# Optimization experiments

Measured on AMD Instinct MI355X. Metric: run time of the kernel, lower is better.

The kernel has to match this reference:

```python
import jax, jax.numpy as jnp
import numpy as np

N_CHANNELS = 270
N_SUBJECTS = 200
B, T = 256, 1024


def setup_inputs() -> dict:
    key = jax.random.key(0)
    k_x, k_s = jax.random.split(key)
    x = jax.random.normal(k_x, (B, N_CHANNELS, T), dtype=jnp.float32)
    subjects = jax.random.randint(k_s, (B,), 0, N_SUBJECTS, dtype=jnp.int64)
    # init_id=True: weights start as identity, then divided by sqrt(C)
    weights = jnp.broadcast_to(jnp.eye(N_CHANNELS, dtype=jnp.float32),
                               (N_SUBJECTS, N_CHANNELS, N_CHANNELS)) / np.sqrt(N_CHANNELS)
    return {"x": x, "subjects": subjects, "weights": weights}


def reference(x, subjects, weights):
    # Gather per-sample CxC weight, then batched matmul: bct,bcd->bdt
    w = weights[subjects]  # (B, C, C)
    return jnp.einsum('bct,bcd->bdt', x, w)
```

## Files before the change

kernel.cpp:

```cpp
#include <hip/hip_runtime.h>


#define C_    270
#define T_    1024
#define B_    256
#define NSUB_ 200

#define BM 96
#define BN 128
#define BK 32
#define NK 9
#define ROWU32 20
#define BOFF (BM * ROWU32)
#define LDSU32 ((BM + BN) * ROWU32)

typedef __attribute__((ext_vector_type(8))) short bf16x8;
typedef __attribute__((ext_vector_type(4))) float f32x4;
typedef __attribute__((ext_vector_type(2))) float f32x2;
typedef __attribute__((ext_vector_type(2))) unsigned u32x2;

__device__ __forceinline__ unsigned pk(float lo, float hi) {
    unsigned a = __builtin_bit_cast(unsigned, lo);
    unsigned b = __builtin_bit_cast(unsigned, hi);
    a += 0x7FFFu + ((a >> 16) & 1u);
    b += 0x7FFFu + ((b >> 16) & 1u);
    return (a >> 16) | (b & 0xFFFF0000u);
}

__device__ __forceinline__ int swz_col(int row, int c2) {
    return (c2 & 3) | ((((c2 >> 2) ^ ((row >> 3) & 3)) & 3) << 2);
}

__global__ __launch_bounds__(256, 4)
void subj_layers_kernel(const float* __restrict__ x,
                        const int* __restrict__ subjects,
                        const float* __restrict__ w,
                        float* __restrict__ out)
{
    __shared__ unsigned lds[2][LDSU32];

    const int tid  = threadIdx.x;
    const int lane = tid & 63;
    const int wid  = tid >> 6;
    const int wr   = wid >> 1;
    const int wc   = wid & 1;
    const int lg   = lane >> 4;
    const int lr   = lane & 15;

    const int bid = blockIdx.x;
    const int b   = bid / 24;
    const int rem = bid % 24;
    const int d0  = (rem >> 3) * BM;
    const int t0  = (rem & 7) * BN;

    int sub = subjects[b];
    sub = sub < 0 ? 0 : (sub >= NSUB_ ? NSUB_ - 1 : sub);
    const float* __restrict__ wsub = w + (size_t)sub * (C_ * C_);
    const float* __restrict__ xb   = x + (size_t)b * (C_ * T_);

    const int btq = tid & 31;
    const int bcq = tid >> 5;
    const int tB  = t0 + 4 * btq;
    const float* __restrict__ xbt = xb + tB;
    const int adp0 = tid % 48,        acq0 = tid / 48;
    const int adp1 = (256 + tid) % 48, acq1 = (256 + tid) / 48;
    const bool hasA1 = (tid < 128);
    const int dA0 = d0 + 2 * adp0;  const bool dA0ok = (dA0 + 1 < C_);
    const int dA1 = d0 + 2 * adp1;  const bool dA1ok = (dA1 + 1 < C_);

    f32x4 acc[3][4];
    #pragma unroll
    for (int m = 0; m < 3; ++m)
        #pragma unroll
        for (int n = 0; n < 4; ++n)
            acc[m][n] = (f32x4){0.f, 0.f, 0.f, 0.f};

    auto load_tiles = [&](int c0, f32x4 pb[4], f32x2 pa0[4], f32x2 pa1[4]) {
        #pragma unroll
        for (int e = 0; e < 4; ++e) {
            const int c = c0 + 4 * bcq + e;
            pb[e] = (c < C_) ? *(const f32x4*)(xbt + (size_t)c * T_)
                             : (f32x4){0.f, 0.f, 0.f, 0.f};
        }
        #pragma unroll
        for (int e = 0; e < 4; ++e) {
            const int c = c0 + 4 * acq0 + e;
            pa0[e] = (dA0ok && c < C_) ? *(const f32x2*)(wsub + (size_t)c * C_ + dA0)
                                       : (f32x2){0.f, 0.f};
        }
        #pragma unroll
        for (int e = 0; e < 4; ++e) {
            const int c = c0 + 4 * acq1 + e;
            pa1[e] = (hasA1 && dA1ok && c < C_) ? *(const f32x2*)(wsub + (size_t)c * C_ + dA1)
                                                : (f32x2){0.f, 0.f};
        }
    };

    auto store_tiles = [&](unsigned* L, const f32x4 pb[4], const f32x2 pa0[4], const f32x2 pa1[4]) {
        unsigned* LB = L + BOFF;
        #pragma unroll
        for (int j = 0; j < 4; ++j) {
            const int r = 4 * btq + j;
            u32x2 v;
            v.x = pk(pb[0][j], pb[1][j]);
            v.y = pk(pb[2][j], pb[3][j]);
            *(u32x2*)(LB + r * ROWU32 + swz_col(r, 2 * bcq)) = v;
        }
        #pragma unroll
        for (int j = 0; j < 2; ++j) {
            const int r = 2 * adp0 + j;
            u32x2 v;
            v.x = pk(pa0[0][j], pa0[1][j]);
            v.y = pk(pa0[2][j], pa0[3][j]);
            *(u32x2*)(L + r * ROWU32 + swz_col(r, 2 * acq0)) = v;
        }
        if (hasA1) {
            #pragma unroll
            for (int j = 0; j < 2; ++j) {
                const int r = 2 * adp1 + j;
                u32x2 v;
                v.x = pk(pa1[0][j], pa1[1][j]);
                v.y = pk(pa1[2][j], pa1[3][j]);
                *(u32x2*)(L + r * ROWU32 + swz_col(r, 2 * acq1)) = v;
            }
        }
    };

    auto compute = [&](const unsigned* L) {
        const unsigned* LB = L + BOFF;
        bf16x8 af[3], bfr[4];
        #pragma unroll
        for (int m = 0; m < 3; ++m) {
            const int row = wr * 48 + m * 16 + lr;
            af[m] = *(const bf16x8*)(L + row * ROWU32 + ((lg ^ ((row >> 3) & 3)) << 2));
        }
        #pragma unroll
        for (int n = 0; n < 4; ++n) {
            const int row = wc * 64 + n * 16 + lr;
            bfr[n] = *(const bf16x8*)(LB + row * ROWU32 + ((lg ^ ((row >> 3) & 3)) << 2));
        }
        #pragma unroll
        for (int m = 0; m < 3; ++m)
            #pragma unroll
            for (int n = 0; n < 4; ++n)
                acc[m][n] = __builtin_amdgcn_mfma_f32_16x16x32_bf16(af[m], bfr[n], acc[m][n], 0, 0, 0);
    };

    {
        f32x4 pb[4]; f32x2 pa0[4], pa1[4];
        load_tiles(0, pb, pa0, pa1);
        store_tiles(&lds[0][0], pb, pa0, pa1);
    }
    __syncthreads();

    int cur = 0;
    #pragma unroll 1
    for (int kk = 0; kk < NK - 1; ++kk) {
        f32x4 pb[4]; f32x2 pa0[4], pa1[4];
        load_tiles((kk + 1) * BK, pb, pa0, pa1);
        compute(&lds[cur][0]);
        store_tiles(&lds[cur ^ 1][0], pb, pa0, pa1);
        __syncthreads();
        cur ^= 1;
    }
    compute(&lds[cur][0]);

    float* outb = out + (size_t)b * (C_ * T_);
    #pragma unroll
    for (int m = 0; m < 3; ++m) {
        const int dbase = d0 + wr * 48 + m * 16 + 4 * lg;
        #pragma unroll
        for (int n = 0; n < 4; ++n) {
            const int t = t0 + wc * 64 + n * 16 + lr;
            #pragma unroll
            for (int rr = 0; rr < 4; ++rr) {
                const int d = dbase + rr;
                if (d < C_)
                    outb[(size_t)d * T_ + t] = acc[m][n][rr];
            }
        }
    }
}

extern "C" void kernel_launch(void* const* d_in, const int* in_sizes, int n_in,
                              void* d_out, int out_size, void* d_ws, size_t ws_size,
                              hipStream_t stream)
{
    const float* x        = (const float*)d_in[0];
    const int*   subjects = (const int*)d_in[1];
    const float* w        = (const float*)d_in[2];
    float* out            = (float*)d_out;

    dim3 grid(B_ * 24);
    dim3 block(256);
    hipLaunchKernelGGL(subj_layers_kernel, grid, block, 0, stream,
                       x, subjects, w, out);
}
```

Measured before the change: 210.6 us.

## Deepen register prefetch, use hardware bf16 convert, remap block order

Replaces the software bf16 rounding with the v_cvt_pk_bf16_f32 instruction. Global loads are now issued two K-steps ahead using two register buffer sets, and bounds checks are skipped on every K-tile except the last. Block IDs are permuted in strides of 8 and the tile order within a batch is changed, likely to spread work across XCDs and improve L2 locality. Launch bounds drop from 4 to 3 blocks per SM to make room for the extra prefetch registers, which risks lower occupancy.

```diff
diff --git a/kernel.cpp b/kernel.cpp
--- a/kernel.cpp
+++ b/kernel.cpp
@@ -20,18 +20,16 @@
 typedef __attribute__((ext_vector_type(2))) unsigned u32x2;
 
 __device__ __forceinline__ unsigned pk(float lo, float hi) {
-    unsigned a = __builtin_bit_cast(unsigned, lo);
-    unsigned b = __builtin_bit_cast(unsigned, hi);
-    a += 0x7FFFu + ((a >> 16) & 1u);
-    b += 0x7FFFu + ((b >> 16) & 1u);
-    return (a >> 16) | (b & 0xFFFF0000u);
+    unsigned r;
+    asm("v_cvt_pk_bf16_f32 %0, %1, %2" : "=v"(r) : "v"(lo), "v"(hi));
+    return r;
 }
 
 __device__ __forceinline__ int swz_col(int row, int c2) {
     return (c2 & 3) | ((((c2 >> 2) ^ ((row >> 3) & 3)) & 3) << 2);
 }
 
-__global__ __launch_bounds__(256, 4)
+__global__ __launch_bounds__(256, 3)
 void subj_layers_kernel(const float* __restrict__ x,
                         const int* __restrict__ subjects,
                         const float* __restrict__ w,
@@ -47,11 +45,11 @@
     const int lg   = lane >> 4;
     const int lr   = lane & 15;
 
-    const int bid = blockIdx.x;
-    const int b   = bid / 24;
-    const int rem = bid % 24;
-    const int d0  = (rem >> 3) * BM;
-    const int t0  = (rem & 7) * BN;
+    const int bid  = (blockIdx.x & 7) * 768 + (blockIdx.x >> 3);
+    const int b    = bid / 24;
+    const int rem  = bid % 24;
+    const int d0   = (rem % 3) * BM;
+    const int t0   = (rem / 3) * BN;
 
     int sub = subjects[b];
     sub = sub < 0 ? 0 : (sub >= NSUB_ ? NSUB_ - 1 : sub);
@@ -60,9 +58,8 @@
 
     const int btq = tid & 31;
     const int bcq = tid >> 5;
-    const int tB  = t0 + 4 * btq;
-    const float* __restrict__ xbt = xb + tB;
-    const int adp0 = tid % 48,        acq0 = tid / 48;
+    const float* __restrict__ xbt = xb + (t0 + 4 * btq);
+    const int adp0 = tid % 48,         acq0 = tid / 48;
     const int adp1 = (256 + tid) % 48, acq1 = (256 + tid) / 48;
     const bool hasA1 = (tid < 128);
     const int dA0 = d0 + 2 * adp0;  const bool dA0ok = (dA0 + 1 < C_);
@@ -75,24 +72,24 @@
         for (int n = 0; n < 4; ++n)
             acc[m][n] = (f32x4){0.f, 0.f, 0.f, 0.f};
 
-    auto load_tiles = [&](int c0, f32x4 pb[4], f32x2 pa0[4], f32x2 pa1[4]) {
+    auto load_tiles = [&](int c0, bool full, f32x4 pb[4], f32x2 pa0[4], f32x2 pa1[4]) {
         #pragma unroll
         for (int e = 0; e < 4; ++e) {
             const int c = c0 + 4 * bcq + e;
-            pb[e] = (c < C_) ? *(const f32x4*)(xbt + (size_t)c * T_)
-                             : (f32x4){0.f, 0.f, 0.f, 0.f};
+            pb[e] = (full || c < C_) ? *(const f32x4*)(xbt + (size_t)c * T_)
+                                     : (f32x4){0.f, 0.f, 0.f, 0.f};
         }
         #pragma unroll
         for (int e = 0; e < 4; ++e) {
             const int c = c0 + 4 * acq0 + e;
-            pa0[e] = (dA0ok && c < C_) ? *(const f32x2*)(wsub + (size_t)c * C_ + dA0)
-                                       : (f32x2){0.f, 0.f};
+            pa0[e] = (dA0ok && (full || c < C_)) ? *(const f32x2*)(wsub + (size_t)c * C_ + dA0)
+                                                 : (f32x2){0.f, 0.f};
         }
         #pragma unroll
         for (int e = 0; e < 4; ++e) {
             const int c = c0 + 4 * acq1 + e;
-            pa1[e] = (hasA1 && dA1ok && c < C_) ? *(const f32x2*)(wsub + (size_t)c * C_ + dA1)
-                                                : (f32x2){0.f, 0.f};
+            pa1[e] = (hasA1 && dA1ok && (full || c < C_)) ? *(const f32x2*)(wsub + (size_t)c * C_ + dA1)
+                                                          : (f32x2){0.f, 0.f};
         }
     };
 
@@ -146,24 +143,33 @@
                 acc[m][n] = __builtin_amdgcn_mfma_f32_16x16x32_bf16(af[m], bfr[n], acc[m][n], 0, 0, 0);
     };
 
-    {
-        f32x4 pb[4]; f32x2 pa0[4], pa1[4];
-        load_tiles(0, pb, pa0, pa1);
-        store_tiles(&lds[0][0], pb, pa0, pa1);
+    f32x4 pbA[4], pbB[4];
+    f32x2 pa0A[4], pa1A[4], pa0B[4], pa1B[4];
+
+    load_tiles(0, true, pbA, pa0A, pa1A);
+    store_tiles(&lds[0][0], pbA, pa0A, pa1A);
+    load_tiles(BK, true, pbB, pa0B, pa1B);
+    __syncthreads();
+
+    #pragma unroll 1
+    for (int kk = 0; kk < 6; kk += 2) {
+        load_tiles((kk + 2) * BK, true, pbA, pa0A, pa1A);
+        compute(&lds[0][0]);
+        store_tiles(&lds[1][0], pbB, pa0B, pa1B);
+        __syncthreads();
+        load_tiles((kk + 3) * BK, true, pbB, pa0B, pa1B);
+        compute(&lds[1][0]);
+        store_tiles(&lds[0][0], pbA, pa0A, pa1A);
+        __syncthreads();
     }
+    load_tiles(8 * BK, false, pbA, pa0A, pa1A);
+    compute(&lds[0][0]);
+    store_tiles(&lds[1][0], pbB, pa0B, pa1B);
     __syncthreads();
-
-    int cur = 0;
-    #pragma unroll 1
-    for (int kk = 0; kk < NK - 1; ++kk) {
-        f32x4 pb[4]; f32x2 pa0[4], pa1[4];
-        load_tiles((kk + 1) * BK, pb, pa0, pa1);
-        compute(&lds[cur][0]);
-        store_tiles(&lds[cur ^ 1][0], pb, pa0, pa1);
-        __syncthreads();
-        cur ^= 1;
-    }
-    compute(&lds[cur][0]);
+    compute(&lds[1][0]);
+    store_tiles(&lds[0][0], pbA, pa0A, pa1A);
+    __syncthreads();
+    compute(&lds[0][0]);
 
     float* outb = out + (size_t)b * (C_ * T_);
     #pragma unroll
```

Measured after the change: 180.3 us. 14.4% less time.
